# Performance work log

Hardware: AMD Instinct MI355X
Metric: run time of the kernel (lower is better)

Reference implementation:

```python
import jax, jax.numpy as jnp
import numpy as np

KS = {0: (6, 18), 1: (4, 12)}


def _build_modal_edges(feat, k_set):
    # feat: [N, C] -> H_modal [N, len(k_set)*N]
    N = feat.shape[0]
    f = feat / jnp.linalg.norm(feat, axis=1, keepdims=True).clip(1e-12)
    sim = f @ f.T  # [N, N] cosine similarity
    H_list = []
    cols_base = jnp.arange(N)
    for k in k_set:
        _, knn = jax.lax.top_k(sim, k + 1)  # [N, k+1]
        rows = knn.reshape(-1)
        cols = jnp.repeat(cols_base, k + 1)
        H = jnp.zeros((N, N), dtype=feat.dtype).at[rows, cols].set(1.0)
        H_list.append(H)
    return jnp.concatenate(H_list, axis=1)


def _build_incidence(feat1, feat2):
    # feat1/feat2: [N, C] (batch-mean features) -> H [2N, 5N]
    N = feat1.shape[0]
    H1 = _build_modal_edges(feat1, KS[0])  # [N, 2N]
    H2 = _build_modal_edges(feat2, KS[1])  # [N, 2N]
    E1, E2 = H1.shape[1], H2.shape[1]
    blk = jnp.concatenate([
        jnp.concatenate([H1, jnp.zeros((N, E2), H1.dtype)], axis=1),
        jnp.concatenate([jnp.zeros((N, E1), H2.dtype), H2], axis=1),
    ], axis=0)  # block_diag -> [2N, 4N]
    eye = jnp.eye(N, dtype=H1.dtype)
    H_inter = jnp.concatenate([eye, eye], axis=0)  # [2N, N]
    return jnp.concatenate([blk, H_inter], axis=1)  # [2N, 5N]


def _hgconv(x, H, W):
    # x: [B, 2N, Fin], H: [2N, E], W: [Fout, Fin] (torch Linear, no bias)
    x = jnp.einsum('bnf,of->bno', x, W)
    DV = H.sum(axis=1).clip(1.0)  # [2N]
    DE = H.sum(axis=0).clip(1.0)  # [E]
    H_norm = H / jnp.sqrt(DV)[:, None] / DE[None, :]
    A = H_norm @ H_norm.T  # [2N, 2N]
    x = jnp.einsum('nm,bmo->bno', A, x)
    return jax.nn.relu(x)


def setup_inputs() -> dict:
    key = jax.random.key(0)
    k1, k2, k3, k4 = jax.random.split(key, 4)
    B, N, C, Hd = 4, 2048, 64, 128
    feat_mod1 = jax.random.normal(k1, (B, N, C), dtype=jnp.float32)
    feat_mod2 = jax.random.normal(k2, (B, N, C), dtype=jnp.float32)
    # xavier_uniform bounds for [out, in]
    b1 = float(np.sqrt(6.0 / (Hd + C)))
    b2 = float(np.sqrt(6.0 / (Hd + Hd)))
    W1 = jax.random.uniform(k3, (Hd, C), minval=-b1, maxval=b1, dtype=jnp.float32)
    W2 = jax.random.uniform(k4, (Hd, Hd), minval=-b2, maxval=b2, dtype=jnp.float32)
    return {"feat_mod1": feat_mod1, "feat_mod2": feat_mod2, "W1": W1, "W2": W2}


def reference(feat_mod1, feat_mod2, W1, W2):
    B, N, _ = feat_mod1.shape
    H = jax.lax.stop_gradient(
        _build_incidence(feat_mod1.mean(axis=0), feat_mod2.mean(axis=0)))
    x = jnp.concatenate([feat_mod1, feat_mod2], axis=1)  # [B, 2N, C]
    x = _hgconv(x, H, W1)
    x = _hgconv(x, H, W2)
    return x[:, :N, :], x[:, N:, :]
```

## Files before the change

### kernel.cpp

```cpp
#include <hip/hip_runtime.h>
#include <math.h>

#define NN 2048
#define TWO_N 4096
#define BB 4
#define CC 64
#define HD 128
#define CANDCAP 32
#define NE4 (4 * NN)


__global__ void k_prep(const float* __restrict__ W1, const float* __restrict__ W2,
                       float* __restrict__ W1T, float* __restrict__ W2T) {
    int id = blockIdx.x * 256 + threadIdx.x;
    if (id < HD * CC) {
        int c = id >> 6, k = id & 63;
        W1T[(size_t)k * HD + c] = W1[id];
    }
    {
        int c = id >> 7, k = id & 127;
        W2T[(size_t)k * HD + c] = W2[id];
    }
}

__global__ void k_mean_norm(const float* __restrict__ f1, const float* __restrict__ f2,
                            float* __restrict__ g32T, double* __restrict__ gR64,
                            int* __restrict__ DV) {
    int n = blockIdx.x;
    int m = blockIdx.y;
    int c = threadIdx.x;
    if (m == 0 && n < 64) DV[n * 64 + c] = 0;
    const float* f = m ? f2 : f1;
    double s = 0.0;
    for (int b = 0; b < BB; ++b) s += (double)f[((size_t)(b * NN) + n) * CC + c];
    double mean = s * 0.25;
    double sq = mean * mean;
    for (int d = 32; d >= 1; d >>= 1) sq += __shfl_xor(sq, d);
    double norm = sqrt(sq);
    if (norm < 1e-12) norm = 1e-12;
    double g = mean / norm;
    g32T[((size_t)m * CC + c) * NN + n] = (float)g;
    gR64[((size_t)m * NN + n) * CC + c] = g;
}

__global__ void __launch_bounds__(256)
k_sims(const float* __restrict__ g32T, float* __restrict__ sims) {
    __shared__ float As[CC][64];
    __shared__ float Bs[CC][64];
    __shared__ float Cs[64][65];
    int m  = blockIdx.y;
    int bi = blockIdx.x >> 5, bj = blockIdx.x & 31;
    if (bi > bj) return;
    int i0 = bi * 64, j0 = bj * 64;
    const float* g = g32T + (size_t)m * CC * NN;
    int tid = threadIdx.x;
    #pragma unroll
    for (int q = 0; q < 16; ++q) {
        int idx = q * 256 + tid;
        int k = idx >> 6, r = idx & 63;
        As[k][r] = g[(size_t)k * NN + i0 + r];
        Bs[k][r] = g[(size_t)k * NN + j0 + r];
    }
    __syncthreads();
    int tr = tid >> 4, tc = tid & 15;
    float acc[4][4] = {{0.f}};
    #pragma unroll
    for (int k = 0; k < CC; ++k) {
        float4 a = *((const float4*)&As[k][tr << 2]);
        float4 b = *((const float4*)&Bs[k][tc << 2]);
        acc[0][0] += a.x * b.x; acc[0][1] += a.x * b.y; acc[0][2] += a.x * b.z; acc[0][3] += a.x * b.w;
        acc[1][0] += a.y * b.x; acc[1][1] += a.y * b.y; acc[1][2] += a.y * b.z; acc[1][3] += a.y * b.w;
        acc[2][0] += a.z * b.x; acc[2][1] += a.z * b.y; acc[2][2] += a.z * b.z; acc[2][3] += a.z * b.w;
        acc[3][0] += a.w * b.x; acc[3][1] += a.w * b.y; acc[3][2] += a.w * b.z; acc[3][3] += a.w * b.w;
    }
    float* srow = sims + (size_t)m * NN * NN;
    #pragma unroll
    for (int x = 0; x < 4; ++x) {
        float4 v = make_float4(acc[x][0], acc[x][1], acc[x][2], acc[x][3]);
        *((float4*)&srow[(size_t)(i0 + (tr << 2) + x) * NN + j0 + (tc << 2)]) = v;
        Cs[(tr << 2) + x][(tc << 2) + 0] = acc[x][0];
        Cs[(tr << 2) + x][(tc << 2) + 1] = acc[x][1];
        Cs[(tr << 2) + x][(tc << 2) + 2] = acc[x][2];
        Cs[(tr << 2) + x][(tc << 2) + 3] = acc[x][3];
    }
    __syncthreads();
    #pragma unroll
    for (int q = 0; q < 4; ++q) {
        int idx = q * 256 + tid;
        int cc = idx >> 4, rr4 = (idx & 15) << 2;
        float4 v = make_float4(Cs[rr4 + 0][cc], Cs[rr4 + 1][cc],
                               Cs[rr4 + 2][cc], Cs[rr4 + 3][cc]);
        *((float4*)&srow[(size_t)(j0 + cc) * NN + i0 + rr4]) = v;
    }
}

__global__ void __launch_bounds__(512)
k_selref(const float* __restrict__ sims, const double* __restrict__ gR64,
         int* __restrict__ knn1, int* __restrict__ knn2, int* __restrict__ DV) {
    __shared__ int    candL[8][CANDCAP];
    __shared__ double dotsL[8][CANDCAP];
    int wave = threadIdx.x >> 6, lane = threadIdx.x & 63;
    int row = blockIdx.x * 8 + wave;
    int m = row >> 11, i = row & 2047;
    int K = m ? 13 : 19;
    const float* s = sims + (size_t)m * NN * NN + (size_t)i * NN;
    float sv[32];
    #pragma unroll
    for (int q = 0; q < 8; ++q) {
        float4 v = *((const float4*)&s[q * 256 + (lane << 2)]);
        sv[q * 4 + 0] = v.x; sv[q * 4 + 1] = v.y; sv[q * 4 + 2] = v.z; sv[q * 4 + 3] = v.w;
    }
    float lo = -1.01f, hi = 1.01f;
    for (int it = 0; it < 15; ++it) {
        float t = 0.5f * (lo + hi);
        int cnt = 0;
        #pragma unroll
        for (int r = 0; r < 32; ++r)
            cnt += __popcll(__ballot(sv[r] >= t));
        if (cnt >= K) lo = t; else hi = t;
    }
    float thr = lo - 1e-5f;
    unsigned long long ltmask = (lane == 0) ? 0ull : ((~0ull) >> (64 - lane));
    int base = 0;
    #pragma unroll
    for (int r = 0; r < 32; ++r) {
        int j = ((r >> 2) << 8) + (lane << 2) + (r & 3);
        bool p = sv[r] >= thr;
        unsigned long long mk = __ballot(p);
        int ofs = base + __popcll(mk & ltmask);
        if (p && ofs < CANDCAP) candL[wave][ofs] = j;
        base += __popcll(mk);
    }
    int cnt = (base < CANDCAP) ? base : CANDCAP;
    __syncthreads();
    const double* gm = gR64 + (size_t)m * NN * CC;
    double qc = gm[(size_t)i * CC + lane];
    int t4 = 0;
    for (; t4 + 3 < cnt; t4 += 4) {
        int j0 = candL[wave][t4 + 0], j1 = candL[wave][t4 + 1];
        int j2 = candL[wave][t4 + 2], j3 = candL[wave][t4 + 3];
        double p0 = qc * gm[(size_t)j0 * CC + lane];
        double p1 = qc * gm[(size_t)j1 * CC + lane];
        double p2 = qc * gm[(size_t)j2 * CC + lane];
        double p3 = qc * gm[(size_t)j3 * CC + lane];
        #pragma unroll
        for (int d = 32; d >= 1; d >>= 1) {
            p0 += __shfl_xor(p0, d); p1 += __shfl_xor(p1, d);
            p2 += __shfl_xor(p2, d); p3 += __shfl_xor(p3, d);
        }
        if (lane == 0) {
            dotsL[wave][t4 + 0] = p0; dotsL[wave][t4 + 1] = p1;
            dotsL[wave][t4 + 2] = p2; dotsL[wave][t4 + 3] = p3;
        }
    }
    for (; t4 < cnt; ++t4) {
        int j = candL[wave][t4];
        double p = qc * gm[(size_t)j * CC + lane];
        #pragma unroll
        for (int d = 32; d >= 1; d >>= 1) p += __shfl_xor(p, d);
        if (lane == 0) dotsL[wave][t4] = p;
    }
    __syncthreads();
    int* knn = m ? knn2 : knn1;
    if (lane < cnt) {
        double vt = dotsL[wave][lane]; int jt = candL[wave][lane];
        int rank = 0;
        for (int s2 = 0; s2 < cnt; ++s2) {
            double vs = dotsL[wave][s2]; int js = candL[wave][s2];
            if (vs > vt || (vs == vt && js < jt)) ++rank;
        }
        if (rank < K) {
            knn[(size_t)i * K + rank] = jt;
            int w = (rank < (m ? 5 : 7)) ? 2 : 1;
            atomicAdd(&DV[m ? NN + jt : jt], w);
        }
    }
}

__global__ void k_scan(const int* __restrict__ DV, int* __restrict__ offs,
                       int* __restrict__ cursor, float* __restrict__ dvisf) {
    int lane = threadIdx.x;
    int base = lane * 64;
    int s = 0;
    for (int q = 0; q < 64; ++q) s += DV[base + q];
    int x = s;
    for (int d = 1; d < 64; d <<= 1) {
        int y = __shfl_up(x, d);
        if (lane >= d) x += y;
    }
    int run = x - s;
    for (int q = 0; q < 64; ++q) {
        int v = base + q;
        offs[v] = run; cursor[v] = run;
        dvisf[v] = (float)(1.0 / sqrt((double)(DV[v] + 1)));
        run += DV[v];
    }
    if (lane == 63) offs[TWO_N] = run;
}

__global__ void k_fill(const int* __restrict__ knn1, const int* __restrict__ knn2,
                       int* __restrict__ cursor, int* __restrict__ entries) {
    int id = blockIdx.x * blockDim.x + threadIdx.x;
    const int M1 = NN * 19, M2 = NN * 13;
    if (id < M1) {
        int i = id / 19, t = id % 19;
        int v = knn1[id];
        int p = atomicAdd(&cursor[v], 1); entries[p] = NN + i;
        if (t < 7) { int p2 = atomicAdd(&cursor[v], 1); entries[p2] = i; }
    } else if (id < M1 + M2) {
        int id2 = id - M1;
        int i = id2 / 13, t = id2 % 13;
        int v = NN + knn2[id2];
        int p = atomicAdd(&cursor[v], 1); entries[p] = 3 * NN + i;
        if (t < 5) { int p2 = atomicAdd(&cursor[v], 1); entries[p2] = 2 * NN + i; }
    }
}

__global__ void k_edgeX(const float4* __restrict__ x1, const float4* __restrict__ x2,
                        const float* __restrict__ dvisf,
                        const int* __restrict__ knn1, const int* __restrict__ knn2,
                        float4* __restrict__ u4) {
    __shared__ int mem[19];
    __shared__ float wv[19];
    int blk = blockIdx.x;
    int t = threadIdx.x;
    int f4 = t & 15, b = t >> 4;
    if (blk < NN) {
        if (t < 19) { int v = knn1[(size_t)blk * 19 + t]; mem[t] = v; wv[t] = dvisf[v]; }
        __syncthreads();
        float ax = 0.f, ay = 0.f, az = 0.f, aw = 0.f;
        #pragma unroll
        for (int q = 0; q < 7; ++q) {
            float w = wv[q];
            float4 val = x1[((size_t)(b * NN) + mem[q]) * 16 + f4];
            ax += val.x * w; ay += val.y * w; az += val.z * w; aw += val.w * w;
        }
        const float i7 = 1.f / 49.f;
        u4[(size_t)blk * 64 + t] = make_float4(ax * i7, ay * i7, az * i7, aw * i7);
        #pragma unroll
        for (int q = 7; q < 19; ++q) {
            float w = wv[q];
            float4 val = x1[((size_t)(b * NN) + mem[q]) * 16 + f4];
            ax += val.x * w; ay += val.y * w; az += val.z * w; aw += val.w * w;
        }
        const float i19 = 1.f / 361.f;
        u4[(size_t)(NN + blk) * 64 + t] =
            make_float4(ax * i19, ay * i19, az * i19, aw * i19);
    } else {
        int i = blk - NN;
        if (t < 13) { int j = knn2[(size_t)i * 13 + t]; mem[t] = j; wv[t] = dvisf[NN + j]; }
        __syncthreads();
        float ax = 0.f, ay = 0.f, az = 0.f, aw = 0.f;
        #pragma unroll
        for (int q = 0; q < 5; ++q) {
            float w = wv[q];
            float4 val = x2[((size_t)(b * NN) + mem[q]) * 16 + f4];
            ax += val.x * w; ay += val.y * w; az += val.z * w; aw += val.w * w;
        }
        const float i5 = 1.f / 25.f;
        u4[(size_t)(2 * NN + i) * 64 + t] =
            make_float4(ax * i5, ay * i5, az * i5, aw * i5);
        #pragma unroll
        for (int q = 5; q < 13; ++q) {
            float w = wv[q];
            float4 val = x2[((size_t)(b * NN) + mem[q]) * 16 + f4];
            ax += val.x * w; ay += val.y * w; az += val.z * w; aw += val.w * w;
        }
        const float i13 = 1.f / 169.f;
        u4[(size_t)(3 * NN + i) * 64 + t] =
            make_float4(ax * i13, ay * i13, az * i13, aw * i13);
    }
}

__global__ void k_nodeX(const float4* __restrict__ u4,
                        const float4* __restrict__ x1, const float4* __restrict__ x2,
                        const float* __restrict__ dvisf,
                        const int* __restrict__ offs, const int* __restrict__ entries,
                        float4* __restrict__ aggx4) {
    int v = blockIdx.x;
    int t = threadIdx.x;
    int f4 = t & 15, b = t >> 4;
    int s = offs[v], e_end = offs[v + 1];
    float a0x = 0.f, a0y = 0.f, a0z = 0.f, a0w = 0.f;
    float a1x = 0.f, a1y = 0.f, a1z = 0.f, a1w = 0.f;
    float a2x = 0.f, a2y = 0.f, a2z = 0.f, a2w = 0.f;
    float a3x = 0.f, a3y = 0.f, a3z = 0.f, a3w = 0.f;
    int p = s;
    for (; p + 3 < e_end; p += 4) {
        int e0 = entries[p], e1 = entries[p + 1], e2 = entries[p + 2], e3 = entries[p + 3];
        float4 v0 = u4[(size_t)e0 * 64 + t];
        float4 v1 = u4[(size_t)e1 * 64 + t];
        float4 v2 = u4[(size_t)e2 * 64 + t];
        float4 v3 = u4[(size_t)e3 * 64 + t];
        a0x += v0.x; a0y += v0.y; a0z += v0.z; a0w += v0.w;
        a1x += v1.x; a1y += v1.y; a1z += v1.z; a1w += v1.w;
        a2x += v2.x; a2y += v2.y; a2z += v2.z; a2w += v2.w;
        a3x += v3.x; a3y += v3.y; a3z += v3.z; a3w += v3.w;
    }
    for (; p < e_end; ++p) {
        float4 v0 = u4[(size_t)entries[p] * 64 + t];
        a0x += v0.x; a0y += v0.y; a0z += v0.z; a0w += v0.w;
    }
    float ax = (a0x + a1x) + (a2x + a3x);
    float ay = (a0y + a1y) + (a2y + a3y);
    float az = (a0z + a1z) + (a2z + a3z);
    float aw = (a0w + a1w) + (a2w + a3w);
    int partner = (v < NN) ? v + NN : v - NN;
    float w0 = dvisf[v], w1 = dvisf[partner];
    float4 xv = (v < NN) ? x1[((size_t)(b * NN) + v) * 16 + f4]
                         : x2[((size_t)(b * NN) + (v - NN)) * 16 + f4];
    float4 xp = (partner < NN) ? x1[((size_t)(b * NN) + partner) * 16 + f4]
                               : x2[((size_t)(b * NN) + (partner - NN)) * 16 + f4];
    ax += 0.25f * (xv.x * w0 + xp.x * w1);
    ay += 0.25f * (xv.y * w0 + xp.y * w1);
    az += 0.25f * (xv.z * w0 + xp.z * w1);
    aw += 0.25f * (xv.w * w0 + xp.w * w1);
    ax *= w0; ay *= w0; az *= w0; aw *= w0;
    aggx4[(size_t)v * 64 + t] = make_float4(ax, ay, az, aw);
}

__global__ void __launch_bounds__(256)
k_gemm1R(const float* __restrict__ aggx, const float* __restrict__ W1T,
         float* __restrict__ z) {
    __shared__ float xT[64][33];
    __shared__ float wT[64][132];
    int tid = threadIdx.x;
    int g0 = blockIdx.x * 32;
    #pragma unroll
    for (int q = 0; q < 8; ++q) {
        int idx = q * 256 + tid;
        int row = idx >> 6, k = idx & 63;
        xT[k][row] = aggx[(size_t)(g0 + row) * CC + k];
    }
    #pragma unroll
    for (int q = 0; q < 32; ++q) {
        int idx = q * 256 + tid;
        wT[idx >> 7][idx & 127] = W1T[idx];
    }
    __syncthreads();
    int tr = tid >> 5, tc = tid & 31;
    int r0 = tr * 4, c0 = tc * 4;
    float acc[4][4] = {{0.f}};
    #pragma unroll
    for (int k = 0; k < CC; ++k) {
        float xr0 = xT[k][r0 + 0], xr1 = xT[k][r0 + 1];
        float xr2 = xT[k][r0 + 2], xr3 = xT[k][r0 + 3];
        float4 w = *((const float4*)&wT[k][c0]);
        acc[0][0] += xr0 * w.x; acc[0][1] += xr0 * w.y; acc[0][2] += xr0 * w.z; acc[0][3] += xr0 * w.w;
        acc[1][0] += xr1 * w.x; acc[1][1] += xr1 * w.y; acc[1][2] += xr1 * w.z; acc[1][3] += xr1 * w.w;
        acc[2][0] += xr2 * w.x; acc[2][1] += xr2 * w.y; acc[2][2] += xr2 * w.z; acc[2][3] += xr2 * w.w;
        acc[3][0] += xr3 * w.x; acc[3][1] += xr3 * w.y; acc[3][2] += xr3 * w.z; acc[3][3] += xr3 * w.w;
    }
    #pragma unroll
    for (int i = 0; i < 4; ++i) {
        float4 v = make_float4(fmaxf(acc[i][0], 0.f), fmaxf(acc[i][1], 0.f),
                               fmaxf(acc[i][2], 0.f), fmaxf(acc[i][3], 0.f));
        *((float4*)&z[(size_t)(g0 + r0 + i) * HD + c0]) = v;
    }
}

__global__ void __launch_bounds__(256)
k_gemm2(const float* __restrict__ zin, const float* __restrict__ W2T,
        float* __restrict__ y) {
    __shared__ float zT[64][33];
    __shared__ float wT[64][132];
    int tid = threadIdx.x;
    int g0 = blockIdx.x * 32;
    int tr = tid >> 5, tc = tid & 31;
    int r0 = tr * 4, c0 = tc * 4;
    float acc[4][4] = {{0.f}};
    for (int kc = 0; kc < 2; ++kc) {
        int k0 = kc * 64;
        __syncthreads();
        #pragma unroll
        for (int q = 0; q < 8; ++q) {
            int idx = q * 256 + tid;
            int row = idx >> 6, k = idx & 63;
            zT[k][row] = zin[(size_t)(g0 + row) * HD + k0 + k];
        }
        #pragma unroll
        for (int q = 0; q < 32; ++q) {
            int idx = q * 256 + tid;
            int k = idx >> 7, c = idx & 127;
            wT[k][c] = W2T[(size_t)(k0 + k) * HD + c];
        }
        __syncthreads();
        #pragma unroll
        for (int k = 0; k < 64; ++k) {
            float zr0 = zT[k][r0 + 0], zr1 = zT[k][r0 + 1];
            float zr2 = zT[k][r0 + 2], zr3 = zT[k][r0 + 3];
            float4 w = *((const float4*)&wT[k][c0]);
            acc[0][0] += zr0 * w.x; acc[0][1] += zr0 * w.y; acc[0][2] += zr0 * w.z; acc[0][3] += zr0 * w.w;
            acc[1][0] += zr1 * w.x; acc[1][1] += zr1 * w.y; acc[1][2] += zr1 * w.z; acc[1][3] += zr1 * w.w;
            acc[2][0] += zr2 * w.x; acc[2][1] += zr2 * w.y; acc[2][2] += zr2 * w.z; acc[2][3] += zr2 * w.w;
            acc[3][0] += zr3 * w.x; acc[3][1] += zr3 * w.y; acc[3][2] += zr3 * w.z; acc[3][3] += zr3 * w.w;
        }
    }
    #pragma unroll
    for (int i = 0; i < 4; ++i) {
        float4 v = make_float4(acc[i][0], acc[i][1], acc[i][2], acc[i][3]);
        *((float4*)&y[(size_t)(g0 + r0 + i) * HD + c0]) = v;
    }
}

__global__ void k_edge(const float4* __restrict__ y4, const float* __restrict__ dvisf,
                       const int* __restrict__ knn1, const int* __restrict__ knn2,
                       float4* __restrict__ u4) {
    __shared__ int mem[19];
    __shared__ float wv[19];
    int blk = blockIdx.x;
    int f4 = threadIdx.x & 31;
    int b  = threadIdx.x >> 5;
    int bo = b * 32 + f4;
    int t = threadIdx.x;
    if (blk < NN) {
        if (t < 19) { int v = knn1[(size_t)blk * 19 + t]; mem[t] = v; wv[t] = dvisf[v]; }
        __syncthreads();
        float ax = 0.f, ay = 0.f, az = 0.f, aw = 0.f;
        #pragma unroll
        for (int q = 0; q < 7; ++q) {
            float w = wv[q];
            float4 val = y4[(size_t)mem[q] * 128 + bo];
            ax += val.x * w; ay += val.y * w; az += val.z * w; aw += val.w * w;
        }
        const float i7 = 1.f / 49.f;
        u4[(size_t)blk * 128 + bo] = make_float4(ax * i7, ay * i7, az * i7, aw * i7);
        #pragma unroll
        for (int q = 7; q < 19; ++q) {
            float w = wv[q];
            float4 val = y4[(size_t)mem[q] * 128 + bo];
            ax += val.x * w; ay += val.y * w; az += val.z * w; aw += val.w * w;
        }
        const float i19 = 1.f / 361.f;
        u4[(size_t)(NN + blk) * 128 + bo] =
            make_float4(ax * i19, ay * i19, az * i19, aw * i19);
    } else {
        int i = blk - NN;
        if (t < 13) { int v = NN + knn2[(size_t)i * 13 + t]; mem[t] = v; wv[t] = dvisf[v]; }
        __syncthreads();
        float ax = 0.f, ay = 0.f, az = 0.f, aw = 0.f;
        #pragma unroll
        for (int q = 0; q < 5; ++q) {
            float w = wv[q];
            float4 val = y4[(size_t)mem[q] * 128 + bo];
            ax += val.x * w; ay += val.y * w; az += val.z * w; aw += val.w * w;
        }
        const float i5 = 1.f / 25.f;
        u4[(size_t)(2 * NN + i) * 128 + bo] =
            make_float4(ax * i5, ay * i5, az * i5, aw * i5);
        #pragma unroll
        for (int q = 5; q < 13; ++q) {
            float w = wv[q];
            float4 val = y4[(size_t)mem[q] * 128 + bo];
            ax += val.x * w; ay += val.y * w; az += val.z * w; aw += val.w * w;
        }
        const float i13 = 1.f / 169.f;
        u4[(size_t)(3 * NN + i) * 128 + bo] =
            make_float4(ax * i13, ay * i13, az * i13, aw * i13);
    }
}

__global__ void k_node2(const float4* __restrict__ u4, const float4* __restrict__ y4,
                        const float* __restrict__ dvisf,
                        const int* __restrict__ offs, const int* __restrict__ entries,
                        float4* __restrict__ outp4) {
    int v = blockIdx.x;
    int f4 = threadIdx.x & 31;
    int b  = threadIdx.x >> 5;
    int bo = b * 32 + f4;
    int s = offs[v], e_end = offs[v + 1];
    float a0x = 0.f, a0y = 0.f, a0z = 0.f, a0w = 0.f;
    float a1x = 0.f, a1y = 0.f, a1z = 0.f, a1w = 0.f;
    float a2x = 0.f, a2y = 0.f, a2z = 0.f, a2w = 0.f;
    float a3x = 0.f, a3y = 0.f, a3z = 0.f, a3w = 0.f;
    int p = s;
    for (; p + 3 < e_end; p += 4) {
        int e0 = entries[p], e1 = entries[p + 1], e2 = entries[p + 2], e3 = entries[p + 3];
        float4 v0 = u4[(size_t)e0 * 128 + bo];
        float4 v1 = u4[(size_t)e1 * 128 + bo];
        float4 v2 = u4[(size_t)e2 * 128 + bo];
        float4 v3 = u4[(size_t)e3 * 128 + bo];
        a0x += v0.x; a0y += v0.y; a0z += v0.z; a0w += v0.w;
        a1x += v1.x; a1y += v1.y; a1z += v1.z; a1w += v1.w;
        a2x += v2.x; a2y += v2.y; a2z += v2.z; a2w += v2.w;
        a3x += v3.x; a3y += v3.y; a3z += v3.z; a3w += v3.w;
    }
    for (; p < e_end; ++p) {
        float4 v0 = u4[(size_t)entries[p] * 128 + bo];
        a0x += v0.x; a0y += v0.y; a0z += v0.z; a0w += v0.w;
    }
    float ax = (a0x + a1x) + (a2x + a3x);
    float ay = (a0y + a1y) + (a2y + a3y);
    float az = (a0z + a1z) + (a2z + a3z);
    float aw = (a0w + a1w) + (a2w + a3w);
    int partner = (v < NN) ? v + NN : v - NN;
    float w0 = dvisf[v], w1 = dvisf[partner];
    float4 yv = y4[(size_t)v * 128 + bo];
    float4 yp = y4[(size_t)partner * 128 + bo];
    ax += 0.25f * (yv.x * w0 + yp.x * w1);
    ay += 0.25f * (yv.y * w0 + yp.y * w1);
    az += 0.25f * (yv.z * w0 + yp.z * w1);
    aw += 0.25f * (yv.w * w0 + yp.w * w1);
    ax *= w0; ay *= w0; az *= w0; aw *= w0;
    float4 res = make_float4(fmaxf(ax, 0.f), fmaxf(ay, 0.f),
                             fmaxf(az, 0.f), fmaxf(aw, 0.f));
    size_t o;
    if (v < NN) o = ((size_t)(b * NN + v)) * 32 + f4;
    else        o = (size_t)BB * NN * 32 + ((size_t)(b * NN + (v - NN))) * 32 + f4;
    outp4[o] = res;
}

extern "C" void kernel_launch(void* const* d_in, const int* in_sizes, int n_in,
                              void* d_out, int out_size, void* d_ws, size_t ws_size,
                              hipStream_t stream) {
    const float* f1 = (const float*)d_in[0];
    const float* f2 = (const float*)d_in[1];
    const float* W1 = (const float*)d_in[2];
    const float* W2 = (const float*)d_in[3];
    float* out = (float*)d_out;

    char* ws = (char*)d_ws;
    size_t off = 0;
    auto alloc = [&](size_t bytes) -> void* {
        void* p = ws + off;
        off = (off + bytes + 255) & ~(size_t)255;
        return p;
    };
    float*  g32T    = (float*)alloc((size_t)2 * CC * NN * 4);
    double* gR64    = (double*)alloc((size_t)2 * NN * CC * 8);
    float*  sims    = (float*)alloc((size_t)2 * NN * NN * 4);
    float*  ybuf    = (float*)alloc((size_t)BB * TWO_N * HD * 4);
    float*  zbuf    = (float*)alloc((size_t)BB * TWO_N * HD * 4);
    float*  ubuf    = (float*)alloc((size_t)BB * NE4 * HD * 4);
    float*  aggx    = (float*)alloc((size_t)BB * TWO_N * CC * 4);
    float*  W1T     = (float*)alloc((size_t)CC * HD * 4);
    float*  W2T     = (float*)alloc((size_t)HD * HD * 4);
    float*  dvisf   = (float*)alloc((size_t)TWO_N * 4);
    int*    knn1    = (int*)alloc((size_t)NN * 19 * 4);
    int*    knn2    = (int*)alloc((size_t)NN * 13 * 4);
    int*    DV      = (int*)alloc((size_t)TWO_N * 4);
    int*    offs    = (int*)alloc((size_t)(TWO_N + 1) * 4);
    int*    cursor  = (int*)alloc((size_t)TWO_N * 4);
    int*    entries = (int*)alloc((size_t)(NN * 26 + NN * 18) * 4);

    k_prep<<<64, 256, 0, stream>>>(W1, W2, W1T, W2T);
    k_mean_norm<<<dim3(NN, 2), 64, 0, stream>>>(f1, f2, g32T, gR64, DV);
    k_sims<<<dim3(32 * 32, 2), 256, 0, stream>>>(g32T, sims);
    k_selref<<<TWO_N / 8, 512, 0, stream>>>(sims, gR64, knn1, knn2, DV);
    k_scan<<<1, 64, 0, stream>>>(DV, offs, cursor, dvisf);
    k_fill<<<(NN * 19 + NN * 13 + 255) / 256, 256, 0, stream>>>(knn1, knn2, cursor, entries);

    k_edgeX<<<2 * NN, 64, 0, stream>>>((const float4*)f1, (const float4*)f2, dvisf,
                                       knn1, knn2, (float4*)ubuf);
    k_nodeX<<<TWO_N, 64, 0, stream>>>((const float4*)ubuf, (const float4*)f1,
                                      (const float4*)f2, dvisf, offs, entries,
                                      (float4*)aggx);
    k_gemm1R<<<(BB * TWO_N) / 32, 256, 0, stream>>>(aggx, W1T, zbuf);

    k_gemm2<<<(BB * TWO_N) / 32, 256, 0, stream>>>(zbuf, W2T, ybuf);
    k_edge<<<2 * NN, 128, 0, stream>>>((const float4*)ybuf, dvisf, knn1, knn2, (float4*)ubuf);
    k_node2<<<TWO_N, 128, 0, stream>>>((const float4*)ubuf, (const float4*)ybuf, dvisf,
                                       offs, entries, (float4*)out);
}
```

Before: 212.6 us.

## Fuse all stages into one persistent kernel with grid barriers and bf16 sims

Replaces the twelve-kernel pipeline with a single persistent kernel of 384 blocks. Stages are separated by hierarchical atomic grid barriers. The similarity matrix is now stored in bf16 to halve its write and read traffic, and the bisection is shortened with a wider candidate margin. Exact fp64 reranking keeps the top-k selection correct. The change removes the per-launch overhead and the gaps between kernels, but adds barrier spin costs, assumes every block is co-resident, and risks ties at the candidate cap.

```diff
diff --git a/kernel.cpp b/kernel.cpp
--- a/kernel.cpp
+++ b/kernel.cpp
@@ -7,507 +7,615 @@
 #define CC 64
 #define HD 128
 #define CANDCAP 32
-#define NE4 (4 * NN)
-
-
-__global__ void k_prep(const float* __restrict__ W1, const float* __restrict__ W2,
-                       float* __restrict__ W1T, float* __restrict__ W2T) {
-    int id = blockIdx.x * 256 + threadIdx.x;
-    if (id < HD * CC) {
-        int c = id >> 6, k = id & 63;
-        W1T[(size_t)k * HD + c] = W1[id];
-    }
-    {
-        int c = id >> 7, k = id & 127;
-        W2T[(size_t)k * HD + c] = W2[id];
-    }
+
+#define NBLK 384
+#define NTHR 512
+#define NWAVES (NBLK * 8)
+
+#define MAGIC0 0x13579BDF
+#define MAGIC1 0x2468ACE1
+
+typedef unsigned short u16;
+
+struct BarMem {
+    int flag[16];
+    int sub[12][8][16];
+    int master[12][16];
+};
+#define BAR_ZERO_DWORDS (12 * 8 * 16 + 12 * 16)
+
+__device__ __forceinline__ void gbar(BarMem* B, int idx) {
+    __syncthreads();
+    if (threadIdx.x == 0) {
+        int line = blockIdx.x & 7;
+        int a = __hip_atomic_fetch_add(&B->sub[idx][line][0], 1,
+                                       __ATOMIC_ACQ_REL, __HIP_MEMORY_SCOPE_AGENT);
+        if (a == (NBLK / 8) - 1)
+            __hip_atomic_fetch_add(&B->master[idx][0], 1,
+                                   __ATOMIC_ACQ_REL, __HIP_MEMORY_SCOPE_AGENT);
+        while (__hip_atomic_load(&B->master[idx][0],
+                                 __ATOMIC_ACQUIRE, __HIP_MEMORY_SCOPE_AGENT) != 8)
+            __builtin_amdgcn_s_sleep(2);
+    }
+    __syncthreads();
 }
 
-__global__ void k_mean_norm(const float* __restrict__ f1, const float* __restrict__ f2,
-                            float* __restrict__ g32T, double* __restrict__ gR64,
-                            int* __restrict__ DV) {
-    int n = blockIdx.x;
-    int m = blockIdx.y;
-    int c = threadIdx.x;
-    if (m == 0 && n < 64) DV[n * 64 + c] = 0;
-    const float* f = m ? f2 : f1;
-    double s = 0.0;
-    for (int b = 0; b < BB; ++b) s += (double)f[((size_t)(b * NN) + n) * CC + c];
-    double mean = s * 0.25;
-    double sq = mean * mean;
-    for (int d = 32; d >= 1; d >>= 1) sq += __shfl_xor(sq, d);
-    double norm = sqrt(sq);
-    if (norm < 1e-12) norm = 1e-12;
-    double g = mean / norm;
-    g32T[((size_t)m * CC + c) * NN + n] = (float)g;
-    gR64[((size_t)m * NN + n) * CC + c] = g;
+__device__ __forceinline__ u16 f2bf(float x) {
+    unsigned u = __float_as_uint(x);
+    u += 0x7FFFu + ((u >> 16) & 1u);
+    return (u16)(u >> 16);
 }
 
-__global__ void __launch_bounds__(256)
-k_sims(const float* __restrict__ g32T, float* __restrict__ sims) {
-    __shared__ float As[CC][64];
-    __shared__ float Bs[CC][64];
-    __shared__ float Cs[64][65];
-    int m  = blockIdx.y;
-    int bi = blockIdx.x >> 5, bj = blockIdx.x & 31;
-    if (bi > bj) return;
-    int i0 = bi * 64, j0 = bj * 64;
-    const float* g = g32T + (size_t)m * CC * NN;
-    int tid = threadIdx.x;
-    #pragma unroll
-    for (int q = 0; q < 16; ++q) {
-        int idx = q * 256 + tid;
-        int k = idx >> 6, r = idx & 63;
-        As[k][r] = g[(size_t)k * NN + i0 + r];
-        Bs[k][r] = g[(size_t)k * NN + j0 + r];
-    }
-    __syncthreads();
-    int tr = tid >> 4, tc = tid & 15;
-    float acc[4][4] = {{0.f}};
-    #pragma unroll
-    for (int k = 0; k < CC; ++k) {
-        float4 a = *((const float4*)&As[k][tr << 2]);
-        float4 b = *((const float4*)&Bs[k][tc << 2]);
-        acc[0][0] += a.x * b.x; acc[0][1] += a.x * b.y; acc[0][2] += a.x * b.z; acc[0][3] += a.x * b.w;
-        acc[1][0] += a.y * b.x; acc[1][1] += a.y * b.y; acc[1][2] += a.y * b.z; acc[1][3] += a.y * b.w;
-        acc[2][0] += a.z * b.x; acc[2][1] += a.z * b.y; acc[2][2] += a.z * b.z; acc[2][3] += a.z * b.w;
-        acc[3][0] += a.w * b.x; acc[3][1] += a.w * b.y; acc[3][2] += a.w * b.z; acc[3][3] += a.w * b.w;
-    }
-    float* srow = sims + (size_t)m * NN * NN;
-    #pragma unroll
-    for (int x = 0; x < 4; ++x) {
-        float4 v = make_float4(acc[x][0], acc[x][1], acc[x][2], acc[x][3]);
-        *((float4*)&srow[(size_t)(i0 + (tr << 2) + x) * NN + j0 + (tc << 2)]) = v;
-        Cs[(tr << 2) + x][(tc << 2) + 0] = acc[x][0];
-        Cs[(tr << 2) + x][(tc << 2) + 1] = acc[x][1];
-        Cs[(tr << 2) + x][(tc << 2) + 2] = acc[x][2];
-        Cs[(tr << 2) + x][(tc << 2) + 3] = acc[x][3];
-    }
-    __syncthreads();
-    #pragma unroll
-    for (int q = 0; q < 4; ++q) {
-        int idx = q * 256 + tid;
-        int cc = idx >> 4, rr4 = (idx & 15) << 2;
-        float4 v = make_float4(Cs[rr4 + 0][cc], Cs[rr4 + 1][cc],
-                               Cs[rr4 + 2][cc], Cs[rr4 + 3][cc]);
-        *((float4*)&srow[(size_t)(j0 + cc) * NN + i0 + rr4]) = v;
-    }
-}
-
-__global__ void __launch_bounds__(512)
-k_selref(const float* __restrict__ sims, const double* __restrict__ gR64,
-         int* __restrict__ knn1, int* __restrict__ knn2, int* __restrict__ DV) {
-    __shared__ int    candL[8][CANDCAP];
-    __shared__ double dotsL[8][CANDCAP];
-    int wave = threadIdx.x >> 6, lane = threadIdx.x & 63;
-    int row = blockIdx.x * 8 + wave;
-    int m = row >> 11, i = row & 2047;
-    int K = m ? 13 : 19;
-    const float* s = sims + (size_t)m * NN * NN + (size_t)i * NN;
-    float sv[32];
-    #pragma unroll
-    for (int q = 0; q < 8; ++q) {
-        float4 v = *((const float4*)&s[q * 256 + (lane << 2)]);
-        sv[q * 4 + 0] = v.x; sv[q * 4 + 1] = v.y; sv[q * 4 + 2] = v.z; sv[q * 4 + 3] = v.w;
-    }
-    float lo = -1.01f, hi = 1.01f;
-    for (int it = 0; it < 15; ++it) {
-        float t = 0.5f * (lo + hi);
-        int cnt = 0;
+__global__ void __launch_bounds__(NTHR, 4)
+k_uber(const float* __restrict__ f1, const float* __restrict__ f2,
+       const float* __restrict__ W1, const float* __restrict__ W2,
+       BarMem* __restrict__ bar,
+       float* __restrict__ g32T, double* __restrict__ gR64,
+       u16* __restrict__ simsbf,
+       float* __restrict__ ybuf, float* __restrict__ zbuf,
+       float* __restrict__ ubuf, float* __restrict__ aggx,
+       float* __restrict__ W1T, float* __restrict__ W2T,
+       float* __restrict__ dvisf,
+       int* __restrict__ knn1, int* __restrict__ knn2,
+       int* __restrict__ DV, int* __restrict__ offs,
+       int* __restrict__ cursor, int* __restrict__ entries,
+       float* __restrict__ out) {
+    __shared__ __align__(16) char SMEM[65536];
+
+    const int tid  = threadIdx.x;
+    const int bid  = blockIdx.x;
+    const int lane = tid & 63;
+    const int wid  = tid >> 6;
+    const int gwave = bid * 8 + wid;
+    const int team = tid >> 8;
+    const int tid2 = tid & 255;
+
+    if (bid == 0) {
+        int* bz = &bar->sub[0][0][0];
+        for (int i = tid; i < BAR_ZERO_DWORDS; i += NTHR) bz[i] = 0;
+        __syncthreads();
+        if (tid == 0) {
+            __hip_atomic_store(&bar->flag[0], MAGIC0, __ATOMIC_RELEASE, __HIP_MEMORY_SCOPE_AGENT);
+            __hip_atomic_store(&bar->flag[1], MAGIC1, __ATOMIC_RELEASE, __HIP_MEMORY_SCOPE_AGENT);
+        }
+    } else {
+        if (tid == 0) {
+            while (__hip_atomic_load(&bar->flag[0], __ATOMIC_ACQUIRE, __HIP_MEMORY_SCOPE_AGENT) != MAGIC0 ||
+                   __hip_atomic_load(&bar->flag[1], __ATOMIC_ACQUIRE, __HIP_MEMORY_SCOPE_AGENT) != MAGIC1)
+                __builtin_amdgcn_s_sleep(2);
+        }
+        __syncthreads();
+    }
+
+    {
+        int gid = bid * NTHR + tid;
+        if (gid < HD * CC) {
+            int c = gid >> 6, k = gid & 63;
+            W1T[(size_t)k * HD + c] = W1[gid];
+        }
+        if (gid < HD * HD) {
+            int c = gid >> 7, k = gid & 127;
+            W2T[(size_t)k * HD + c] = W2[gid];
+        }
+        if (gid < TWO_N) DV[gid] = 0;
+
+        for (int rowt = gwave; rowt < TWO_N; rowt += NWAVES) {
+            int m = rowt >> 11, n = rowt & 2047;
+            const float* f = m ? f2 : f1;
+            double s = 0.0;
+            for (int b = 0; b < BB; ++b)
+                s += (double)f[((size_t)(b * NN) + n) * CC + lane];
+            double mean = s * 0.25;
+            double sq = mean * mean;
+            for (int d = 32; d >= 1; d >>= 1) sq += __shfl_xor(sq, d);
+            double norm = sqrt(sq);
+            if (norm < 1e-12) norm = 1e-12;
+            double gg = mean / norm;
+            g32T[((size_t)m * CC + lane) * NN + n] = (float)gg;
+            gR64[((size_t)m * NN + n) * CC + lane] = gg;
+        }
+    }
+    gbar(bar, 0);
+
+    {
+        for (int itr = 0; itr < 2; ++itr) {
+            int tile = bid * 2 + team + itr * (NBLK * 2);
+            bool act = tile < 1056;
+            int m = 0, bi = 0, bj = 0;
+            if (act) {
+                m = tile >= 528 ? 1 : 0;
+                int r = tile - m * 528;
+                while (r >= 32 - bi) { r -= 32 - bi; ++bi; }
+                bj = bi + r;
+            }
+            float* As = (float*)(SMEM + (size_t)team * 32768);
+            float* Bs = As + 4096;
+            int i0 = bi * 64, j0 = bj * 64;
+            const float* g = g32T + (size_t)m * CC * NN;
+            if (act) {
+                #pragma unroll
+                for (int q = 0; q < 16; ++q) {
+                    int idx = q * 256 + tid2;
+                    int k = idx >> 6, rr = idx & 63;
+                    As[k * 64 + rr] = g[(size_t)k * NN + i0 + rr];
+                    Bs[k * 64 + rr] = g[(size_t)k * NN + j0 + rr];
+                }
+            }
+            __syncthreads();
+            float acc[4][4] = {{0.f}};
+            int tr = tid2 >> 4, tc = tid2 & 15;
+            if (act) {
+                #pragma unroll
+                for (int k = 0; k < CC; ++k) {
+                    float4 a = *((const float4*)&As[k * 64 + (tr << 2)]);
+                    float4 b = *((const float4*)&Bs[k * 64 + (tc << 2)]);
+                    acc[0][0] += a.x * b.x; acc[0][1] += a.x * b.y; acc[0][2] += a.x * b.z; acc[0][3] += a.x * b.w;
+                    acc[1][0] += a.y * b.x; acc[1][1] += a.y * b.y; acc[1][2] += a.y * b.z; acc[1][3] += a.y * b.w;
+                    acc[2][0] += a.z * b.x; acc[2][1] += a.z * b.y; acc[2][2] += a.z * b.z; acc[2][3] += a.z * b.w;
+                    acc[3][0] += a.w * b.x; acc[3][1] += a.w * b.y; acc[3][2] += a.w * b.z; acc[3][3] += a.w * b.w;
+                }
+            }
+            __syncthreads();
+            u16* Cs = (u16*)As;
+            u16* srow = simsbf + (size_t)m * NN * NN;
+            if (act) {
+                #pragma unroll
+                for (int x = 0; x < 4; ++x) {
+                    ushort4 vd;
+                    vd.x = f2bf(acc[x][0]); vd.y = f2bf(acc[x][1]);
+                    vd.z = f2bf(acc[x][2]); vd.w = f2bf(acc[x][3]);
+                    *((ushort4*)&srow[(size_t)(i0 + (tr << 2) + x) * NN + j0 + (tc << 2)]) = vd;
+                    int cr = ((tr << 2) + x) * 66 + (tc << 2);
+                    Cs[cr + 0] = vd.x; Cs[cr + 1] = vd.y;
+                    Cs[cr + 2] = vd.z; Cs[cr + 3] = vd.w;
+                }
+            }
+            __syncthreads();
+            if (act) {
+                #pragma unroll
+                for (int q = 0; q < 4; ++q) {
+                    int idx = q * 256 + tid2;
+                    int cc = idx >> 4, rr4 = (idx & 15) << 2;
+                    ushort4 vd;
+                    vd.x = Cs[(rr4 + 0) * 66 + cc];
+                    vd.y = Cs[(rr4 + 1) * 66 + cc];
+                    vd.z = Cs[(rr4 + 2) * 66 + cc];
+                    vd.w = Cs[(rr4 + 3) * 66 + cc];
+                    *((ushort4*)&srow[(size_t)(j0 + cc) * NN + i0 + rr4]) = vd;
+                }
+            }
+            __syncthreads();
+        }
+    }
+    gbar(bar, 1);
+
+    {
+        int* candL = (int*)(SMEM + (size_t)wid * 384);
+        double* dotsL = (double*)(SMEM + (size_t)wid * 384 + 128);
+        for (int row = gwave; row < TWO_N; row += NWAVES) {
+            int m = row >> 11, i = row & 2047;
+            int K = m ? 13 : 19;
+            const u16* s = simsbf + (size_t)m * NN * NN + (size_t)i * NN;
+            float sv[32];
+            #pragma unroll
+            for (int q = 0; q < 4; ++q) {
+                uint4 w = *((const uint4*)(s + q * 512 + (lane << 3)));
+                sv[q*8+0] = __uint_as_float(w.x << 16);
+                sv[q*8+1] = __uint_as_float(w.x & 0xFFFF0000u);
+                sv[q*8+2] = __uint_as_float(w.y << 16);
+                sv[q*8+3] = __uint_as_float(w.y & 0xFFFF0000u);
+                sv[q*8+4] = __uint_as_float(w.z << 16);
+                sv[q*8+5] = __uint_as_float(w.z & 0xFFFF0000u);
+                sv[q*8+6] = __uint_as_float(w.w << 16);
+                sv[q*8+7] = __uint_as_float(w.w & 0xFFFF0000u);
+            }
+            float lo = -1.01f, hi = 1.01f;
+            for (int it = 0; it < 12; ++it) {
+                float t = 0.5f * (lo + hi);
+                int c = 0;
+                #pragma unroll
+                for (int r = 0; r < 32; ++r)
+                    c += __popcll(__ballot(sv[r] >= t));
+                if (c >= K) lo = t; else hi = t;
+            }
+            float thr = lo - 6e-3f;
+            unsigned long long ltmask = (lane == 0) ? 0ull : ((~0ull) >> (64 - lane));
+            int base = 0;
+            #pragma unroll
+            for (int r = 0; r < 32; ++r) {
+                int j = ((r >> 3) << 9) + (lane << 3) + (r & 7);
+                bool p = sv[r] >= thr;
+                unsigned long long mk = __ballot(p);
+                int ofs = base + __popcll(mk & ltmask);
+                if (p && ofs < CANDCAP) candL[ofs] = j;
+                base += __popcll(mk);
+            }
+            int cnt = (base < CANDCAP) ? base : CANDCAP;
+            __threadfence_block();
+            const double* gm = gR64 + (size_t)m * NN * CC;
+            double qc = gm[(size_t)i * CC + lane];
+            int t4 = 0;
+            for (; t4 + 3 < cnt; t4 += 4) {
+                int j0c = candL[t4 + 0], j1c = candL[t4 + 1];
+                int j2c = candL[t4 + 2], j3c = candL[t4 + 3];
+                double p0 = qc * gm[(size_t)j0c * CC + lane];
+                double p1 = qc * gm[(size_t)j1c * CC + lane];
+                double p2 = qc * gm[(size_t)j2c * CC + lane];
+                double p3 = qc * gm[(size_t)j3c * CC + lane];
+                #pragma unroll
+                for (int d = 32; d >= 1; d >>= 1) {
+                    p0 += __shfl_xor(p0, d); p1 += __shfl_xor(p1, d);
+                    p2 += __shfl_xor(p2, d); p3 += __shfl_xor(p3, d);
+                }
+                if (lane == 0) {
+                    dotsL[t4 + 0] = p0; dotsL[t4 + 1] = p1;
+                    dotsL[t4 + 2] = p2; dotsL[t4 + 3] = p3;
+                }
+            }
+            for (; t4 < cnt; ++t4) {
+                int j = candL[t4];
+                double p = qc * gm[(size_t)j * CC + lane];
+                #pragma unroll
+                for (int d = 32; d >= 1; d >>= 1) p += __shfl_xor(p, d);
+                if (lane == 0) dotsL[t4] = p;
+            }
+            __threadfence_block();
+            int* knn = m ? knn2 : knn1;
+            if (lane < cnt) {
+                double vt = dotsL[lane]; int jt = candL[lane];
+                int rank = 0;
+                for (int s2 = 0; s2 < cnt; ++s2) {
+                    double vs = dotsL[s2]; int js = candL[s2];
+                    if (vs > vt || (vs == vt && js < jt)) ++rank;
+                }
+                if (rank < K) {
+                    knn[(size_t)i * K + rank] = jt;
+                    int w = (rank < (m ? 5 : 7)) ? 2 : 1;
+                    atomicAdd(&DV[m ? NN + jt : jt], w);
+                }
+            }
+            __threadfence_block();
+        }
+    }
+    gbar(bar, 2);
+
+    if (bid == 0 && tid < 64) {
+        int ln = tid;
+        int base = ln * 64;
+        int s = 0;
+        for (int q = 0; q < 64; ++q) s += DV[base + q];
+        int x = s;
+        for (int d = 1; d < 64; d <<= 1) {
+            int y = __shfl_up(x, d);
+            if (ln >= d) x += y;
+        }
+        int run = x - s;
+        for (int q = 0; q < 64; ++q) {
+            int v = base + q;
+            offs[v] = run; cursor[v] = run;
+            dvisf[v] = (float)(1.0 / sqrt((double)(DV[v] + 1)));
+            run += DV[v];
+        }
+        if (ln == 63) offs[TWO_N] = run;
+    }
+    gbar(bar, 3);
+
+    {
+        int gid = bid * NTHR + tid;
+        const int M1 = NN * 19, M2 = NN * 13;
+        if (gid < M1) {
+            int i = gid / 19, t = gid % 19;
+            int v = knn1[gid];
+            int p = atomicAdd(&cursor[v], 1); entries[p] = NN + i;
+            if (t < 7) { int p2 = atomicAdd(&cursor[v], 1); entries[p2] = i; }
+        } else if (gid < M1 + M2) {
+            int id2 = gid - M1;
+            int i = id2 / 13, t = id2 % 13;
+            int v = NN + knn2[id2];
+            int p = atomicAdd(&cursor[v], 1); entries[p] = 3 * NN + i;
+            if (t < 5) { int p2 = atomicAdd(&cursor[v], 1); entries[p2] = 2 * NN + i; }
+        }
+
+        const float4* x1 = (const float4*)f1;
+        const float4* x2 = (const float4*)f2;
+        float4* u4 = (float4*)ubuf;
+        for (int pt = gwave; pt < TWO_N; pt += NWAVES) {
+            int ff = lane & 15, b = lane >> 4;
+            if (pt < NN) {
+                int mv = 0; float wv = 0.f;
+                if (lane < 19) { mv = knn1[(size_t)pt * 19 + lane]; wv = dvisf[mv]; }
+                float ax = 0.f, ay = 0.f, az = 0.f, aw = 0.f;
+                #pragma unroll
+                for (int q = 0; q < 7; ++q) {
+                    int mq = __shfl(mv, q); float wq = __shfl(wv, q);
+                    float4 val = x1[((size_t)(b * NN) + mq) * 16 + ff];
+                    ax += val.x * wq; ay += val.y * wq; az += val.z * wq; aw += val.w * wq;
+                }
+                u4[(size_t)pt * 64 + lane] =
+                    make_float4(ax * (1.f/49.f), ay * (1.f/49.f), az * (1.f/49.f), aw * (1.f/49.f));
+                #pragma unroll
+                for (int q = 7; q < 19; ++q) {
+                    int mq = __shfl(mv, q); float wq = __shfl(wv, q);
+                    float4 val = x1[((size_t)(b * NN) + mq) * 16 + ff];
+                    ax += val.x * wq; ay += val.y * wq; az += val.z * wq; aw += val.w * wq;
+                }
+                u4[(size_t)(NN + pt) * 64 + lane] =
+                    make_float4(ax * (1.f/361.f), ay * (1.f/361.f), az * (1.f/361.f), aw * (1.f/361.f));
+            } else {
+                int i = pt - NN;
+                int mv = 0; float wv = 0.f;
+                if (lane < 13) { mv = knn2[(size_t)i * 13 + lane]; wv = dvisf[NN + mv]; }
+                float ax = 0.f, ay = 0.f, az = 0.f, aw = 0.f;
+                #pragma unroll
+                for (int q = 0; q < 5; ++q) {
+                    int mq = __shfl(mv, q); float wq = __shfl(wv, q);
+                    float4 val = x2[((size_t)(b * NN) + mq) * 16 + ff];
+                    ax += val.x * wq; ay += val.y * wq; az += val.z * wq; aw += val.w * wq;
+                }
+                u4[(size_t)(2 * NN + i) * 64 + lane] =
+                    make_float4(ax * (1.f/25.f), ay * (1.f/25.f), az * (1.f/25.f), aw * (1.f/25.f));
+                #pragma unroll
+                for (int q = 5; q < 13; ++q) {
+                    int mq = __shfl(mv, q); float wq = __shfl(wv, q);
+                    float4 val = x2[((size_t)(b * NN) + mq) * 16 + ff];
+                    ax += val.x * wq; ay += val.y * wq; az += val.z * wq; aw += val.w * wq;
+                }
+                u4[(size_t)(3 * NN + i) * 64 + lane] =
+                    make_float4(ax * (1.f/169.f), ay * (1.f/169.f), az * (1.f/169.f), aw * (1.f/169.f));
+            }
+        }
+    }
+    gbar(bar, 4);
+
+    {
+        const float4* u4 = (const float4*)ubuf;
+        const float4* x1 = (const float4*)f1;
+        const float4* x2 = (const float4*)f2;
+        float4* aggx4 = (float4*)aggx;
+        for (int v = gwave; v < TWO_N; v += NWAVES) {
+            int ff = lane & 15, b = lane >> 4;
+            int s = offs[v], e_end = offs[v + 1];
+            float a0x=0,a0y=0,a0z=0,a0w=0, a1x=0,a1y=0,a1z=0,a1w=0;
+            float a2x=0,a2y=0,a2z=0,a2w=0, a3x=0,a3y=0,a3z=0,a3w=0;
+            int p = s;
+            for (; p + 3 < e_end; p += 4) {
+                int e0 = entries[p], e1 = entries[p+1], e2 = entries[p+2], e3 = entries[p+3];
+                float4 v0 = u4[(size_t)e0 * 64 + lane];
+                float4 v1 = u4[(size_t)e1 * 64 + lane];
+                float4 v2 = u4[(size_t)e2 * 64 + lane];
+                float4 v3 = u4[(size_t)e3 * 64 + lane];
+                a0x+=v0.x;a0y+=v0.y;a0z+=v0.z;a0w+=v0.w;
+                a1x+=v1.x;a1y+=v1.y;a1z+=v1.z;a1w+=v1.w;
+                a2x+=v2.x;a2y+=v2.y;a2z+=v2.z;a2w+=v2.w;
+                a3x+=v3.x;a3y+=v3.y;a3z+=v3.z;a3w+=v3.w;
+            }
+            for (; p < e_end; ++p) {
+                float4 v0 = u4[(size_t)entries[p] * 64 + lane];
+                a0x+=v0.x;a0y+=v0.y;a0z+=v0.z;a0w+=v0.w;
+            }
+            float ax = (a0x+a1x)+(a2x+a3x);
+            float ay = (a0y+a1y)+(a2y+a3y);
+            float az = (a0z+a1z)+(a2z+a3z);
+            float aw = (a0w+a1w)+(a2w+a3w);
+            int partner = (v < NN) ? v + NN : v - NN;
+            float w0 = dvisf[v], w1 = dvisf[partner];
+            float4 xv = (v < NN) ? x1[((size_t)(b*NN) + v) * 16 + ff]
+                                 : x2[((size_t)(b*NN) + (v - NN)) * 16 + ff];
+            float4 xp = (partner < NN) ? x1[((size_t)(b*NN) + partner) * 16 + ff]
+                                       : x2[((size_t)(b*NN) + (partner - NN)) * 16 + ff];
+            ax += 0.25f * (xv.x * w0 + xp.x * w1);
+            ay += 0.25f * (xv.y * w0 + xp.y * w1);
+            az += 0.25f * (xv.z * w0 + xp.z * w1);
+            aw += 0.25f * (xv.w * w0 + xp.w * w1);
+            ax *= w0; ay *= w0; az *= w0; aw *= w0;
+            aggx4[(size_t)v * 64 + lane] = make_float4(ax, ay, az, aw);
+        }
+    }
+    gbar(bar, 5);
+
+    {
+        float* wT = (float*)SMEM;
+        float* xT = ((float*)(SMEM + 33792)) + team * 2112;
         #pragma unroll
-        for (int r = 0; r < 32; ++r)
-            cnt += __popcll(__ballot(sv[r] >= t));
-        if (cnt >= K) lo = t; else hi = t;
-    }
-    float thr = lo - 1e-5f;
-    unsigned long long ltmask = (lane == 0) ? 0ull : ((~0ull) >> (64 - lane));
-    int base = 0;
-    #pragma unroll
-    for (int r = 0; r < 32; ++r) {
-        int j = ((r >> 2) << 8) + (lane << 2) + (r & 3);
-        bool p = sv[r] >= thr;
-        unsigned long long mk = __ballot(p);
-        int ofs = base + __popcll(mk & ltmask);
-        if (p && ofs < CANDCAP) candL[wave][ofs] = j;
-        base += __popcll(mk);
-    }
-    int cnt = (base < CANDCAP) ? base : CANDCAP;
-    __syncthreads();
-    const double* gm = gR64 + (size_t)m * NN * CC;
-    double qc = gm[(size_t)i * CC + lane];
-    int t4 = 0;
-    for (; t4 + 3 < cnt; t4 += 4) {
-        int j0 = candL[wave][t4 + 0], j1 = candL[wave][t4 + 1];
-        int j2 = candL[wave][t4 + 2], j3 = candL[wave][t4 + 3];
-        double p0 = qc * gm[(size_t)j0 * CC + lane];
-        double p1 = qc * gm[(size_t)j1 * CC + lane];
-        double p2 = qc * gm[(size_t)j2 * CC + lane];
-        double p3 = qc * gm[(size_t)j3 * CC + lane];
-        #pragma unroll
-        for (int d = 32; d >= 1; d >>= 1) {
-            p0 += __shfl_xor(p0, d); p1 += __shfl_xor(p1, d);
-            p2 += __shfl_xor(p2, d); p3 += __shfl_xor(p3, d);
-        }
-        if (lane == 0) {
-            dotsL[wave][t4 + 0] = p0; dotsL[wave][t4 + 1] = p1;
-            dotsL[wave][t4 + 2] = p2; dotsL[wave][t4 + 3] = p3;
-        }
-    }
-    for (; t4 < cnt; ++t4) {
-        int j = candL[wave][t4];
-        double p = qc * gm[(size_t)j * CC + lane];
-        #pragma unroll
-        for (int d = 32; d >= 1; d >>= 1) p += __shfl_xor(p, d);
-        if (lane == 0) dotsL[wave][t4] = p;
-    }
-    __syncthreads();
-    int* knn = m ? knn2 : knn1;
-    if (lane < cnt) {
-        double vt = dotsL[wave][lane]; int jt = candL[wave][lane];
-        int rank = 0;
-        for (int s2 = 0; s2 < cnt; ++s2) {
-            double vs = dotsL[wave][s2]; int js = candL[wave][s2];
-            if (vs > vt || (vs == vt && js < jt)) ++rank;
-        }
-        if (rank < K) {
-            knn[(size_t)i * K + rank] = jt;
-            int w = (rank < (m ? 5 : 7)) ? 2 : 1;
-            atomicAdd(&DV[m ? NN + jt : jt], w);
-        }
-    }
-}
-
-__global__ void k_scan(const int* __restrict__ DV, int* __restrict__ offs,
-                       int* __restrict__ cursor, float* __restrict__ dvisf) {
-    int lane = threadIdx.x;
-    int base = lane * 64;
-    int s = 0;
-    for (int q = 0; q < 64; ++q) s += DV[base + q];
-    int x = s;
-    for (int d = 1; d < 64; d <<= 1) {
-        int y = __shfl_up(x, d);
-        if (lane >= d) x += y;
-    }
-    int run = x - s;
-    for (int q = 0; q < 64; ++q) {
-        int v = base + q;
-        offs[v] = run; cursor[v] = run;
-        dvisf[v] = (float)(1.0 / sqrt((double)(DV[v] + 1)));
-        run += DV[v];
-    }
-    if (lane == 63) offs[TWO_N] = run;
-}
-
-__global__ void k_fill(const int* __restrict__ knn1, const int* __restrict__ knn2,
-                       int* __restrict__ cursor, int* __restrict__ entries) {
-    int id = blockIdx.x * blockDim.x + threadIdx.x;
-    const int M1 = NN * 19, M2 = NN * 13;
-    if (id < M1) {
-        int i = id / 19, t = id % 19;
-        int v = knn1[id];
-        int p = atomicAdd(&cursor[v], 1); entries[p] = NN + i;
-        if (t < 7) { int p2 = atomicAdd(&cursor[v], 1); entries[p2] = i; }
-    } else if (id < M1 + M2) {
-        int id2 = id - M1;
-        int i = id2 / 13, t = id2 % 13;
-        int v = NN + knn2[id2];
-        int p = atomicAdd(&cursor[v], 1); entries[p] = 3 * NN + i;
-        if (t < 5) { int p2 = atomicAdd(&cursor[v], 1); entries[p2] = 2 * NN + i; }
-    }
-}
-
-__global__ void k_edgeX(const float4* __restrict__ x1, const float4* __restrict__ x2,
-                        const float* __restrict__ dvisf,
-                        const int* __restrict__ knn1, const int* __restrict__ knn2,
-                        float4* __restrict__ u4) {
-    __shared__ int mem[19];
-    __shared__ float wv[19];
-    int blk = blockIdx.x;
-    int t = threadIdx.x;
-    int f4 = t & 15, b = t >> 4;
-    if (blk < NN) {
-        if (t < 19) { int v = knn1[(size_t)blk * 19 + t]; mem[t] = v; wv[t] = dvisf[v]; }
+        for (int p = 0; p < 16; ++p) {
+            int idx = p * NTHR + tid;
+            wT[(idx >> 7) * 132 + (idx & 127)] = W1T[idx];
+        }
+        int gteam = bid * 2 + team;
+        bool act = gteam < (BB * TWO_N) / 32;
+        int g0 = gteam * 32;
+        if (act) {
+            #pragma unroll
+            for (int q = 0; q < 8; ++q) {
+                int idx = q * 256 + tid2;
+                int row = idx >> 6, k = idx & 63;
+                xT[k * 33 + row] = aggx[(size_t)(g0 + row) * CC + k];
+            }
+        }
         __syncthreads();
-        float ax = 0.f, ay = 0.f, az = 0.f, aw = 0.f;
-        #pragma unroll
-        for (int q = 0; q < 7; ++q) {
-            float w = wv[q];
-            float4 val = x1[((size_t)(b * NN) + mem[q]) * 16 + f4];
-            ax += val.x * w; ay += val.y * w; az += val.z * w; aw += val.w * w;
-        }
-        const float i7 = 1.f / 49.f;
-        u4[(size_t)blk * 64 + t] = make_float4(ax * i7, ay * i7, az * i7, aw * i7);
-        #pragma unroll
-        for (int q = 7; q < 19; ++q) {
-            float w = wv[q];
-            float4 val = x1[((size_t)(b * NN) + mem[q]) * 16 + f4];
-            ax += val.x * w; ay += val.y * w; az += val.z * w; aw += val.w * w;
-        }
-        const float i19 = 1.f / 361.f;
-        u4[(size_t)(NN + blk) * 64 + t] =
-            make_float4(ax * i19, ay * i19, az * i19, aw * i19);
-    } else {
-        int i = blk - NN;
-        if (t < 13) { int j = knn2[(size_t)i * 13 + t]; mem[t] = j; wv[t] = dvisf[NN + j]; }
-        __syncthreads();
-        float ax = 0.f, ay = 0.f, az = 0.f, aw = 0.f;
-        #pragma unroll
-        for (int q = 0; q < 5; ++q) {
-            float w = wv[q];
-            float4 val = x2[((size_t)(b * NN) + mem[q]) * 16 + f4];
-            ax += val.x * w; ay += val.y * w; az += val.z * w; aw += val.w * w;
-        }
-        const float i5 = 1.f / 25.f;
-        u4[(size_t)(2 * NN + i) * 64 + t] =
-            make_float4(ax * i5, ay * i5, az * i5, aw * i5);
-        #pragma unroll
-        for (int q = 5; q < 13; ++q) {
-            float w = wv[q];
-            float4 val = x2[((size_t)(b * NN) + mem[q]) * 16 + f4];
-            ax += val.x * w; ay += val.y * w; az += val.z * w; aw += val.w * w;
-        }
-        const float i13 = 1.f / 169.f;
-        u4[(size_t)(3 * NN + i) * 64 + t] =
-            make_float4(ax * i13, ay * i13, az * i13, aw * i13);
-    }
-}
-
-__global__ void k_nodeX(const float4* __restrict__ u4,
-                        const float4* __restrict__ x1, const float4* __restrict__ x2,
-                        const float* __restrict__ dvisf,
-                        const int* __restrict__ offs, const int* __restrict__ entries,
-                        float4* __restrict__ aggx4) {
-    int v = blockIdx.x;
-    int t = threadIdx.x;
-    int f4 = t & 15, b = t >> 4;
-    int s = offs[v], e_end = offs[v + 1];
-    float a0x = 0.f, a0y = 0.f, a0z = 0.f, a0w = 0.f;
-    float a1x = 0.f, a1y = 0.f, a1z = 0.f, a1w = 0.f;
-    float a2x = 0.f, a2y = 0.f, a2z = 0.f, a2w = 0.f;
-    float a3x = 0.f, a3y = 0.f, a3z = 0.f, a3w = 0.f;
-    int p = s;
-    for (; p + 3 < e_end; p += 4) {
-        int e0 = entries[p], e1 = entries[p + 1], e2 = entries[p + 2], e3 = entries[p + 3];
-        float4 v0 = u4[(size_t)e0 * 64 + t];
-        float4 v1 = u4[(size_t)e1 * 64 + t];
-        float4 v2 = u4[(size_t)e2 * 64 + t];
-        float4 v3 = u4[(size_t)e3 * 64 + t];
-        a0x += v0.x; a0y += v0.y; a0z += v0.z; a0w += v0.w;
-        a1x += v1.x; a1y += v1.y; a1z += v1.z; a1w += v1.w;
-        a2x += v2.x; a2y += v2.y; a2z += v2.z; a2w += v2.w;
-        a3x += v3.x; a3y += v3.y; a3z += v3.z; a3w += v3.w;
-    }
-    for (; p < e_end; ++p) {
-        float4 v0 = u4[(size_t)entries[p] * 64 + t];
-        a0x += v0.x; a0y += v0.y; a0z += v0.z; a0w += v0.w;
-    }
-    float ax = (a0x + a1x) + (a2x + a3x);
-    float ay = (a0y + a1y) + (a2y + a3y);
-    float az = (a0z + a1z) + (a2z + a3z);
-    float aw = (a0w + a1w) + (a2w + a3w);
-    int partner = (v < NN) ? v + NN : v - NN;
-    float w0 = dvisf[v], w1 = dvisf[partner];
-    float4 xv = (v < NN) ? x1[((size_t)(b * NN) + v) * 16 + f4]
-                         : x2[((size_t)(b * NN) + (v - NN)) * 16 + f4];
-    float4 xp = (partner < NN) ? x1[((size_t)(b * NN) + partner) * 16 + f4]
-                               : x2[((size_t)(b * NN) + (partner - NN)) * 16 + f4];
-    ax += 0.25f * (xv.x * w0 + xp.x * w1);
-    ay += 0.25f * (xv.y * w0 + xp.y * w1);
-    az += 0.25f * (xv.z * w0 + xp.z * w1);
-    aw += 0.25f * (xv.w * w0 + xp.w * w1);
-    ax *= w0; ay *= w0; az *= w0; aw *= w0;
-    aggx4[(size_t)v * 64 + t] = make_float4(ax, ay, az, aw);
-}
-
-__global__ void __launch_bounds__(256)
-k_gemm1R(const float* __restrict__ aggx, const float* __restrict__ W1T,
-         float* __restrict__ z) {
-    __shared__ float xT[64][33];
-    __shared__ float wT[64][132];
-    int tid = threadIdx.x;
-    int g0 = blockIdx.x * 32;
-    #pragma unroll
-    for (int q = 0; q < 8; ++q) {
-        int idx = q * 256 + tid;
-        int row = idx >> 6, k = idx & 63;
-        xT[k][row] = aggx[(size_t)(g0 + row) * CC + k];
-    }
-    #pragma unroll
-    for (int q = 0; q < 32; ++q) {
-        int idx = q * 256 + tid;
-        wT[idx >> 7][idx & 127] = W1T[idx];
-    }
-    __syncthreads();
-    int tr = tid >> 5, tc = tid & 31;
-    int r0 = tr * 4, c0 = tc * 4;
-    float acc[4][4] = {{0.f}};
-    #pragma unroll
-    for (int k = 0; k < CC; ++k) {
-        float xr0 = xT[k][r0 + 0], xr1 = xT[k][r0 + 1];
-        float xr2 = xT[k][r0 + 2], xr3 = xT[k][r0 + 3];
-        float4 w = *((const float4*)&wT[k][c0]);
-        acc[0][0] += xr0 * w.x; acc[0][1] += xr0 * w.y; acc[0][2] += xr0 * w.z; acc[0][3] += xr0 * w.w;
-        acc[1][0] += xr1 * w.x; acc[1][1] += xr1 * w.y; acc[1][2] += xr1 * w.z; acc[1][3] += xr1 * w.w;
-        acc[2][0] += xr2 * w.x; acc[2][1] += xr2 * w.y; acc[2][2] += xr2 * w.z; acc[2][3] += xr2 * w.w;
-        acc[3][0] += xr3 * w.x; acc[3][1] += xr3 * w.y; acc[3][2] += xr3 * w.z; acc[3][3] += xr3 * w.w;
-    }
-    #pragma unroll
-    for (int i = 0; i < 4; ++i) {
-        float4 v = make_float4(fmaxf(acc[i][0], 0.f), fmaxf(acc[i][1], 0.f),
-                               fmaxf(acc[i][2], 0.f), fmaxf(acc[i][3], 0.f));
-        *((float4*)&z[(size_t)(g0 + r0 + i) * HD + c0]) = v;
-    }
-}
-
-__global__ void __launch_bounds__(256)
-k_gemm2(const float* __restrict__ zin, const float* __restrict__ W2T,
-        float* __restrict__ y) {
-    __shared__ float zT[64][33];
-    __shared__ float wT[64][132];
-    int tid = threadIdx.x;
-    int g0 = blockIdx.x * 32;
-    int tr = tid >> 5, tc = tid & 31;
-    int r0 = tr * 4, c0 = tc * 4;
-    float acc[4][4] = {{0.f}};
-    for (int kc = 0; kc < 2; ++kc) {
-        int k0 = kc * 64;
-        __syncthreads();
-        #pragma unroll
-        for (int q = 0; q < 8; ++q) {
-            int idx = q * 256 + tid;
-            int row = idx >> 6, k = idx & 63;
-            zT[k][row] = zin[(size_t)(g0 + row) * HD + k0 + k];
-        }
-        #pragma unroll
-        for (int q = 0; q < 32; ++q) {
-            int idx = q * 256 + tid;
-            int k = idx >> 7, c = idx & 127;
-            wT[k][c] = W2T[(size_t)(k0 + k) * HD + c];
-        }
-        __syncthreads();
-        #pragma unroll
-        for (int k = 0; k < 64; ++k) {
-            float zr0 = zT[k][r0 + 0], zr1 = zT[k][r0 + 1];
-            float zr2 = zT[k][r0 + 2], zr3 = zT[k][r0 + 3];
-            float4 w = *((const float4*)&wT[k][c0]);
-            acc[0][0] += zr0 * w.x; acc[0][1] += zr0 * w.y; acc[0][2] += zr0 * w.z; acc[0][3] += zr0 * w.w;
-            acc[1][0] += zr1 * w.x; acc[1][1] += zr1 * w.y; acc[1][2] += zr1 * w.z; acc[1][3] += zr1 * w.w;
-            acc[2][0] += zr2 * w.x; acc[2][1] += zr2 * w.y; acc[2][2] += zr2 * w.z; acc[2][3] += zr2 * w.w;
-            acc[3][0] += zr3 * w.x; acc[3][1] += zr3 * w.y; acc[3][2] += zr3 * w.z; acc[3][3] += zr3 * w.w;
-        }
-    }
-    #pragma unroll
-    for (int i = 0; i < 4; ++i) {
-        float4 v = make_float4(acc[i][0], acc[i][1], acc[i][2], acc[i][3]);
-        *((float4*)&y[(size_t)(g0 + r0 + i) * HD + c0]) = v;
-    }
-}
-
-__global__ void k_edge(const float4* __restrict__ y4, const float* __restrict__ dvisf,
-                       const int* __restrict__ knn1, const int* __restrict__ knn2,
-                       float4* __restrict__ u4) {
-    __shared__ int mem[19];
-    __shared__ float wv[19];
-    int blk = blockIdx.x;
-    int f4 = threadIdx.x & 31;
-    int b  = threadIdx.x >> 5;
-    int bo = b * 32 + f4;
-    int t = threadIdx.x;
-    if (blk < NN) {
-        if (t < 19) { int v = knn1[(size_t)blk * 19 + t]; mem[t] = v; wv[t] = dvisf[v]; }
-        __syncthreads();
-        float ax = 0.f, ay = 0.f, az = 0.f, aw = 0.f;
-        #pragma unroll
-        for (int q = 0; q < 7; ++q) {
-            float w = wv[q];
-            float4 val = y4[(size_t)mem[q] * 128 + bo];
-            ax += val.x * w; ay += val.y * w; az += val.z * w; aw += val.w * w;
-        }
-        const float i7 = 1.f / 49.f;
-        u4[(size_t)blk * 128 + bo] = make_float4(ax * i7, ay * i7, az * i7, aw * i7);
-        #pragma unroll
-        for (int q = 7; q < 19; ++q) {
-            float w = wv[q];
-            float4 val = y4[(size_t)mem[q] * 128 + bo];
-            ax += val.x * w; ay += val.y * w; az += val.z * w; aw += val.w * w;
-        }
-        const float i19 = 1.f / 361.f;
-        u4[(size_t)(NN + blk) * 128 + bo] =
-            make_float4(ax * i19, ay * i19, az * i19, aw * i19);
-    } else {
-        int i = blk - NN;
-        if (t < 13) { int v = NN + knn2[(size_t)i * 13 + t]; mem[t] = v; wv[t] = dvisf[v]; }
-        __syncthreads();
-        float ax = 0.f, ay = 0.f, az = 0.f, aw = 0.f;
-        #pragma unroll
-        for (int q = 0; q < 5; ++q) {
-            float w = wv[q];
-            float4 val = y4[(size_t)mem[q] * 128 + bo];
-            ax += val.x * w; ay += val.y * w; az += val.z * w; aw += val.w * w;
-        }
-        const float i5 = 1.f / 25.f;
-        u4[(size_t)(2 * NN + i) * 128 + bo] =
-            make_float4(ax * i5, ay * i5, az * i5, aw * i5);
-        #pragma unroll
-        for (int q = 5; q < 13; ++q) {
-            float w = wv[q];
-            float4 val = y4[(size_t)mem[q] * 128 + bo];
-            ax += val.x * w; ay += val.y * w; az += val.z * w; aw += val.w * w;
-        }
-        const float i13 = 1.f / 169.f;
-        u4[(size_t)(3 * NN + i) * 128 + bo] =
-            make_float4(ax * i13, ay * i13, az * i13, aw * i13);
-    }
-}
-
-__global__ void k_node2(const float4* __restrict__ u4, const float4* __restrict__ y4,
-                        const float* __restrict__ dvisf,
-                        const int* __restrict__ offs, const int* __restrict__ entries,
-                        float4* __restrict__ outp4) {
-    int v = blockIdx.x;
-    int f4 = threadIdx.x & 31;
-    int b  = threadIdx.x >> 5;
-    int bo = b * 32 + f4;
-    int s = offs[v], e_end = offs[v + 1];
-    float a0x = 0.f, a0y = 0.f, a0z = 0.f, a0w = 0.f;
-    float a1x = 0.f, a1y = 0.f, a1z = 0.f, a1w = 0.f;
-    float a2x = 0.f, a2y = 0.f, a2z = 0.f, a2w = 0.f;
-    float a3x = 0.f, a3y = 0.f, a3z = 0.f, a3w = 0.f;
-    int p = s;
-    for (; p + 3 < e_end; p += 4) {
-        int e0 = entries[p], e1 = entries[p + 1], e2 = entries[p + 2], e3 = entries[p + 3];
-        float4 v0 = u4[(size_t)e0 * 128 + bo];
-        float4 v1 = u4[(size_t)e1 * 128 + bo];
-        float4 v2 = u4[(size_t)e2 * 128 + bo];
-        float4 v3 = u4[(size_t)e3 * 128 + bo];
-        a0x += v0.x; a0y += v0.y; a0z += v0.z; a0w += v0.w;
-        a1x += v1.x; a1y += v1.y; a1z += v1.z; a1w += v1.w;
-        a2x += v2.x; a2y += v2.y; a2z += v2.z; a2w += v2.w;
-        a3x += v3.x; a3y += v3.y; a3z += v3.z; a3w += v3.w;
-    }
-    for (; p < e_end; ++p) {
-        float4 v0 = u4[(size_t)entries[p] * 128 + bo];
-        a0x += v0.x; a0y += v0.y; a0z += v0.z; a0w += v0.w;
-    }
-    float ax = (a0x + a1x) + (a2x + a3x);
-    float ay = (a0y + a1y) + (a2y + a3y);
-    float az = (a0z + a1z) + (a2z + a3z);
-    float aw = (a0w + a1w) + (a2w + a3w);
-    int partner = (v < NN) ? v + NN : v - NN;
-    float w0 = dvisf[v], w1 = dvisf[partner];
-    float4 yv = y4[(size_t)v * 128 + bo];
-    float4 yp = y4[(size_t)partner * 128 + bo];
-    ax += 0.25f * (yv.x * w0 + yp.x * w1);
-    ay += 0.25f * (yv.y * w0 + yp.y * w1);
-    az += 0.25f * (yv.z * w0 + yp.z * w1);
-    aw += 0.25f * (yv.w * w0 + yp.w * w1);
-    ax *= w0; ay *= w0; az *= w0; aw *= w0;
-    float4 res = make_float4(fmaxf(ax, 0.f), fmaxf(ay, 0.f),
-                             fmaxf(az, 0.f), fmaxf(aw, 0.f));
-    size_t o;
-    if (v < NN) o = ((size_t)(b * NN + v)) * 32 + f4;
-    else        o = (size_t)BB * NN * 32 + ((size_t)(b * NN + (v - NN))) * 32 + f4;
-    outp4[o] = res;
+        if (act) {
+            int tr = tid2 >> 5, tc = tid2 & 31;
+            int r0 = tr * 4, c0 = tc * 4;
+            float acc[4][4] = {{0.f}};
+            #pragma unroll
+            for (int k = 0; k < CC; ++k) {
+                float xr0 = xT[k*33 + r0+0], xr1 = xT[k*33 + r0+1];
+                float xr2 = xT[k*33 + r0+2], xr3 = xT[k*33 + r0+3];
+                float4 w = *((const float4*)&wT[k * 132 + c0]);
+                acc[0][0]+=xr0*w.x; acc[0][1]+=xr0*w.y; acc[0][2]+=xr0*w.z; acc[0][3]+=xr0*w.w;
+                acc[1][0]+=xr1*w.x; acc[1][1]+=xr1*w.y; acc[1][2]+=xr1*w.z; acc[1][3]+=xr1*w.w;
+                acc[2][0]+=xr2*w.x; acc[2][1]+=xr2*w.y; acc[2][2]+=xr2*w.z; acc[2][3]+=xr2*w.w;
+                acc[3][0]+=xr3*w.x; acc[3][1]+=xr3*w.y; acc[3][2]+=xr3*w.z; acc[3][3]+=xr3*w.w;
+            }
+            #pragma unroll
+            for (int i = 0; i < 4; ++i) {
+                float4 v = make_float4(fmaxf(acc[i][0],0.f), fmaxf(acc[i][1],0.f),
+                                       fmaxf(acc[i][2],0.f), fmaxf(acc[i][3],0.f));
+                *((float4*)&zbuf[(size_t)(g0 + r0 + i) * HD + c0]) = v;
+            }
+        }
+    }
+    gbar(bar, 6);
+
+    {
+        float* wT = (float*)SMEM;
+        float* zT = ((float*)(SMEM + 33792)) + team * 2112;
+        int gteam = bid * 2 + team;
+        bool act = gteam < (BB * TWO_N) / 32;
+        int g0 = gteam * 32;
+        int tr = tid2 >> 5, tc = tid2 & 31;
+        int r0 = tr * 4, c0 = tc * 4;
+        float acc[4][4] = {{0.f}};
+        for (int kc = 0; kc < 2; ++kc) {
+            __syncthreads();
+            #pragma unroll
+            for (int p = 0; p < 16; ++p) {
+                int idx = p * NTHR + tid;
+                int k = idx >> 7, c = idx & 127;
+                wT[k * 132 + c] = W2T[(size_t)(kc * 64 + k) * HD + c];
+            }
+            if (act) {
+                #pragma unroll
+                for (int q = 0; q < 8; ++q) {
+                    int idx = q * 256 + tid2;
+                    int row = idx >> 6, k = idx & 63;
+                    zT[k * 33 + row] = zbuf[(size_t)(g0 + row) * HD + kc * 64 + k];
+                }
+            }
+            __syncthreads();
+            if (act) {
+                #pragma unroll
+                for (int k = 0; k < 64; ++k) {
+                    float zr0 = zT[k*33 + r0+0], zr1 = zT[k*33 + r0+1];
+                    float zr2 = zT[k*33 + r0+2], zr3 = zT[k*33 + r0+3];
+                    float4 w = *((const float4*)&wT[k * 132 + c0]);
+                    acc[0][0]+=zr0*w.x; acc[0][1]+=zr0*w.y; acc[0][2]+=zr0*w.z; acc[0][3]+=zr0*w.w;
+                    acc[1][0]+=zr1*w.x; acc[1][1]+=zr1*w.y; acc[1][2]+=zr1*w.z; acc[1][3]+=zr1*w.w;
+                    acc[2][0]+=zr2*w.x; acc[2][1]+=zr2*w.y; acc[2][2]+=zr2*w.z; acc[2][3]+=zr2*w.w;
+                    acc[3][0]+=zr3*w.x; acc[3][1]+=zr3*w.y; acc[3][2]+=zr3*w.z; acc[3][3]+=zr3*w.w;
+                }
+            }
+        }
+        if (act) {
+            #pragma unroll
+            for (int i = 0; i < 4; ++i) {
+                float4 v = make_float4(acc[i][0], acc[i][1], acc[i][2], acc[i][3]);
+                *((float4*)&ybuf[(size_t)(g0 + r0 + i) * HD + c0]) = v;
+            }
+        }
+    }
+    gbar(bar, 7);
+
+    {
+        const float4* y4 = (const float4*)ybuf;
+        float4* u4 = (float4*)ubuf;
+        int wteam = wid >> 1, wsub = wid & 1;
+        int gt2 = bid * 4 + wteam;
+        for (int pt = gt2; pt < TWO_N; pt += NBLK * 4) {
+            int ff = lane & 31;
+            int b = wsub * 2 + (lane >> 5);
+            int bo = b * 32 + ff;
+            if (pt < NN) {
+                int mv = 0; float wv = 0.f;
+                if (lane < 19) { mv = knn1[(size_t)pt * 19 + lane]; wv = dvisf[mv]; }
+                float ax=0,ay=0,az=0,aw=0;
+                #pragma unroll
+                for (int q = 0; q < 7; ++q) {
+                    int mq = __shfl(mv, q); float wq = __shfl(wv, q);
+                    float4 val = y4[(size_t)mq * 128 + bo];
+                    ax += val.x*wq; ay += val.y*wq; az += val.z*wq; aw += val.w*wq;
+                }
+                u4[(size_t)pt * 128 + bo] =
+                    make_float4(ax*(1.f/49.f), ay*(1.f/49.f), az*(1.f/49.f), aw*(1.f/49.f));
+                #pragma unroll
+                for (int q = 7; q < 19; ++q) {
+                    int mq = __shfl(mv, q); float wq = __shfl(wv, q);
+                    float4 val = y4[(size_t)mq * 128 + bo];
+                    ax += val.x*wq; ay += val.y*wq; az += val.z*wq; aw += val.w*wq;
+                }
+                u4[(size_t)(NN + pt) * 128 + bo] =
+                    make_float4(ax*(1.f/361.f), ay*(1.f/361.f), az*(1.f/361.f), aw*(1.f/361.f));
+            } else {
+                int i = pt - NN;
+                int mv = 0; float wv = 0.f;
+                if (lane < 13) { mv = NN + knn2[(size_t)i * 13 + lane]; wv = dvisf[mv]; }
+                float ax=0,ay=0,az=0,aw=0;
+                #pragma unroll
+                for (int q = 0; q < 5; ++q) {
+                    int mq = __shfl(mv, q); float wq = __shfl(wv, q);
+                    float4 val = y4[(size_t)mq * 128 + bo];
+                    ax += val.x*wq; ay += val.y*wq; az += val.z*wq; aw += val.w*wq;
+                }
+                u4[(size_t)(2 * NN + i) * 128 + bo] =
+                    make_float4(ax*(1.f/25.f), ay*(1.f/25.f), az*(1.f/25.f), aw*(1.f/25.f));
+                #pragma unroll
+                for (int q = 5; q < 13; ++q) {
+                    int mq = __shfl(mv, q); float wq = __shfl(wv, q);
+                    float4 val = y4[(size_t)mq * 128 + bo];
+                    ax += val.x*wq; ay += val.y*wq; az += val.z*wq; aw += val.w*wq;
+                }
+                u4[(size_t)(3 * NN + i) * 128 + bo] =
+                    make_float4(ax*(1.f/169.f), ay*(1.f/169.f), az*(1.f/169.f), aw*(1.f/169.f));
+            }
+        }
+    }
+    gbar(bar, 8);
+
+    {
+        const float4* u4 = (const float4*)ubuf;
+        const float4* y4 = (const float4*)ybuf;
+        float4* outp4 = (float4*)out;
+        int wteam = wid >> 1, wsub = wid & 1;
+        int gt2 = bid * 4 + wteam;
+        for (int v = gt2; v < TWO_N; v += NBLK * 4) {
+            int ff = lane & 31;
+            int b = wsub * 2 + (lane >> 5);
+            int bo = b * 32 + ff;
+            int s = offs[v], e_end = offs[v + 1];
+            float a0x=0,a0y=0,a0z=0,a0w=0, a1x=0,a1y=0,a1z=0,a1w=0;
+            float a2x=0,a2y=0,a2z=0,a2w=0, a3x=0,a3y=0,a3z=0,a3w=0;
+            int p = s;
+            for (; p + 3 < e_end; p += 4) {
+                int e0 = entries[p], e1 = entries[p+1], e2 = entries[p+2], e3 = entries[p+3];
+                float4 v0 = u4[(size_t)e0 * 128 + bo];
+                float4 v1 = u4[(size_t)e1 * 128 + bo];
+                float4 v2 = u4[(size_t)e2 * 128 + bo];
+                float4 v3 = u4[(size_t)e3 * 128 + bo];
+                a0x+=v0.x;a0y+=v0.y;a0z+=v0.z;a0w+=v0.w;
+                a1x+=v1.x;a1y+=v1.y;a1z+=v1.z;a1w+=v1.w;
+                a2x+=v2.x;a2y+=v2.y;a2z+=v2.z;a2w+=v2.w;
+                a3x+=v3.x;a3y+=v3.y;a3z+=v3.z;a3w+=v3.w;
+            }
+            for (; p < e_end; ++p) {
+                float4 v0 = u4[(size_t)entries[p] * 128 + bo];
+                a0x+=v0.x;a0y+=v0.y;a0z+=v0.z;a0w+=v0.w;
+            }
+            float ax = (a0x+a1x)+(a2x+a3x);
+            float ay = (a0y+a1y)+(a2y+a3y);
+            float az = (a0z+a1z)+(a2z+a3z);
+            float aw = (a0w+a1w)+(a2w+a3w);
+            int partner = (v < NN) ? v + NN : v - NN;
+            float w0 = dvisf[v], w1 = dvisf[partner];
+            float4 yv = y4[(size_t)v * 128 + bo];
+            float4 yp = y4[(size_t)partner * 128 + bo];
+            ax += 0.25f * (yv.x * w0 + yp.x * w1);
+            ay += 0.25f * (yv.y * w0 + yp.y * w1);
+            az += 0.25f * (yv.z * w0 + yp.z * w1);
+            aw += 0.25f * (yv.w * w0 + yp.w * w1);
+            ax *= w0; ay *= w0; az *= w0; aw *= w0;
+            float4 res = make_float4(fmaxf(ax,0.f), fmaxf(ay,0.f),
+                                     fmaxf(az,0.f), fmaxf(aw,0.f));
+            size_t o;
+            if (v < NN) o = ((size_t)(b * NN + v)) * 32 + ff;
+            else        o = (size_t)BB * NN * 32 + ((size_t)(b * NN + (v - NN))) * 32 + ff;
+            outp4[o] = res;
+        }
+    }
+
+    if (bid == 0 && tid == 0) {
+        __hip_atomic_store(&bar->flag[0], 0, __ATOMIC_RELEASE, __HIP_MEMORY_SCOPE_AGENT);
+        __hip_atomic_store(&bar->flag[1], 0, __ATOMIC_RELEASE, __HIP_MEMORY_SCOPE_AGENT);
+    }
 }
 
 extern "C" void kernel_launch(void* const* d_in, const int* in_sizes, int n_in,
@@ -526,39 +634,25 @@
         off = (off + bytes + 255) & ~(size_t)255;
         return p;
     };
-    float*  g32T    = (float*)alloc((size_t)2 * CC * NN * 4);
-    double* gR64    = (double*)alloc((size_t)2 * NN * CC * 8);
-    float*  sims    = (float*)alloc((size_t)2 * NN * NN * 4);
-    float*  ybuf    = (float*)alloc((size_t)BB * TWO_N * HD * 4);
-    float*  zbuf    = (float*)alloc((size_t)BB * TWO_N * HD * 4);
-    float*  ubuf    = (float*)alloc((size_t)BB * NE4 * HD * 4);
-    float*  aggx    = (float*)alloc((size_t)BB * TWO_N * CC * 4);
-    float*  W1T     = (float*)alloc((size_t)CC * HD * 4);
-    float*  W2T     = (float*)alloc((size_t)HD * HD * 4);
-    float*  dvisf   = (float*)alloc((size_t)TWO_N * 4);
-    int*    knn1    = (int*)alloc((size_t)NN * 19 * 4);
-    int*    knn2    = (int*)alloc((size_t)NN * 13 * 4);
-    int*    DV      = (int*)alloc((size_t)TWO_N * 4);
-    int*    offs    = (int*)alloc((size_t)(TWO_N + 1) * 4);
-    int*    cursor  = (int*)alloc((size_t)TWO_N * 4);
-    int*    entries = (int*)alloc((size_t)(NN * 26 + NN * 18) * 4);
-
-    k_prep<<<64, 256, 0, stream>>>(W1, W2, W1T, W2T);
-    k_mean_norm<<<dim3(NN, 2), 64, 0, stream>>>(f1, f2, g32T, gR64, DV);
-    k_sims<<<dim3(32 * 32, 2), 256, 0, stream>>>(g32T, sims);
-    k_selref<<<TWO_N / 8, 512, 0, stream>>>(sims, gR64, knn1, knn2, DV);
-    k_scan<<<1, 64, 0, stream>>>(DV, offs, cursor, dvisf);
-    k_fill<<<(NN * 19 + NN * 13 + 255) / 256, 256, 0, stream>>>(knn1, knn2, cursor, entries);
-
-    k_edgeX<<<2 * NN, 64, 0, stream>>>((const float4*)f1, (const float4*)f2, dvisf,
-                                       knn1, knn2, (float4*)ubuf);
-    k_nodeX<<<TWO_N, 64, 0, stream>>>((const float4*)ubuf, (const float4*)f1,
-                                      (const float4*)f2, dvisf, offs, entries,
-                                      (float4*)aggx);
-    k_gemm1R<<<(BB * TWO_N) / 32, 256, 0, stream>>>(aggx, W1T, zbuf);
-
-    k_gemm2<<<(BB * TWO_N) / 32, 256, 0, stream>>>(zbuf, W2T, ybuf);
-    k_edge<<<2 * NN, 128, 0, stream>>>((const float4*)ybuf, dvisf, knn1, knn2, (float4*)ubuf);
-    k_node2<<<TWO_N, 128, 0, stream>>>((const float4*)ubuf, (const float4*)ybuf, dvisf,
-                                       offs, entries, (float4*)out);
+    BarMem* bar    = (BarMem*)alloc(sizeof(BarMem));
+    float*  g32T   = (float*)alloc((size_t)2 * CC * NN * 4);
+    double* gR64   = (double*)alloc((size_t)2 * NN * CC * 8);
+    u16*    simsbf = (u16*)alloc((size_t)2 * NN * NN * 2);
+    float*  ybuf   = (float*)alloc((size_t)BB * TWO_N * HD * 4);
+    float*  zbuf   = (float*)alloc((size_t)BB * TWO_N * HD * 4);
+    float*  ubuf   = (float*)alloc((size_t)BB * 4 * NN * HD * 4);
+    float*  aggx   = (float*)alloc((size_t)BB * TWO_N * CC * 4);
+    float*  W1T    = (float*)alloc((size_t)CC * HD * 4);
+    float*  W2T    = (float*)alloc((size_t)HD * HD * 4);
+    float*  dvisf  = (float*)alloc((size_t)TWO_N * 4);
+    int*    knn1   = (int*)alloc((size_t)NN * 19 * 4);
+    int*    knn2   = (int*)alloc((size_t)NN * 13 * 4);
+    int*    DV     = (int*)alloc((size_t)TWO_N * 4);
+    int*    offs   = (int*)alloc((size_t)(TWO_N + 1) * 4);
+    int*    cursor = (int*)alloc((size_t)TWO_N * 4);
+    int*    entries= (int*)alloc((size_t)(NN * 26 + NN * 18) * 4);
+
+    k_uber<<<dim3(NBLK), dim3(NTHR), 0, stream>>>(
+        f1, f2, W1, W2, bar, g32T, gR64, simsbf, ybuf, zbuf, ubuf, aggx,
+        W1T, W2T, dvisf, knn1, knn2, DV, offs, cursor, entries, out);
 }
```

After: 776.5 us. 265% more time.
